# Performance work log

Measured on AMD Instinct MI355X. Metric: run time of the kernel, lower is better.

The kernel has to match this reference:

```python
import jax, jax.numpy as jnp
import numpy as np

PATCH = (1, 5, 5)   # NN_patch_size (t, h, w)
CHUNK = 3600


def unfold3d_patches(video):
    """video: [B,C,T,H,W] -> [N, d] overlapping (1,5,5) patches, stride 1, VALID.
    d = C*1*5*5; N = B*T*(H-4)*(W-4). Element order within d is consistent
    across calls, which is all the L2 KNN + MSE math requires."""
    p = jax.lax.conv_general_dilated_patches(
        video, filter_shape=PATCH, window_strides=(1, 1, 1), padding='VALID')
    # p: [B, C*prod(PATCH), T', H', W']
    d = p.shape[1]
    return jnp.moveaxis(p, 1, -1).reshape(-1, d)


def knn_argmin(q, k):
    """Exact 1-NN under L2 (faiss IndexFlatL2 equivalent), chunked over queries."""
    kn = jnp.sum(k * k, axis=1)                      # [Nk]
    qc = q.reshape(-1, CHUNK, q.shape[1])            # [nchunks, CHUNK, d]

    def one_chunk(qb):
        qn = jnp.sum(qb * qb, axis=1, keepdims=True)  # [CHUNK,1]
        d2 = qn + kn[None, :] - 2.0 * (qb @ k.T)      # [CHUNK, Nk]
        return jnp.argmin(d2, axis=1)

    return jax.lax.map(one_chunk, qc).reshape(-1)    # [Nq]


def setup_inputs() -> dict:
    key = jax.random.key(0)
    k1, k2 = jax.random.split(key)
    shape = (1, 3, 4, 64, 64)  # [B,C,T,H,W]
    return {
        'result': jax.random.normal(k1, shape, dtype=jnp.float32),
        'valid_video': jax.random.normal(k2, shape, dtype=jnp.float32),
    }


def reference(result, valid_video):
    q = unfold3d_patches(result)        # [Nq, 75] query patches
    k = unfold3d_patches(valid_video)   # [Nk, 75] valid (key/value) patches
    idx = knn_argmin(q, k)              # [Nq] nearest valid patch per query
    nn = k[idx]                         # gather (F.embedding equivalent)
    # nn.MSELoss(reduction='sum')
    diff = q - nn
    return jnp.sum(diff * diff)
```

## Files before the change

### kernel.cpp

```cpp
#include <hip/hip_runtime.h>
#include <hip/hip_bf16.h>
#include <math.h>

typedef __attribute__((ext_vector_type(8))) short bf16x8;
typedef __attribute__((ext_vector_type(4))) float f32x4;
typedef unsigned short ushort_t;

#define NP 14400
#define NS 5
#define NIT 45
#define TILEB 12288

__device__ __forceinline__ ushort_t f2bf(float f) {
  unsigned u = __float_as_uint(f);
  u += 0x7FFF + ((u >> 16) & 1);
  return (ushort_t)(u >> 16);
}
__device__ __forceinline__ float bf2f(ushort_t b) {
  return __uint_as_float(((unsigned)b) << 16);
}

__device__ __forceinline__ size_t kidx(int p, int d) {
  return ((size_t)(((p >> 6) * 12 + ((p >> 4) & 3) * 3 + (d >> 5)) * 64
          + ((d >> 3) & 3) * 16 + (p & 15))) * 8 + (d & 7);
}
__device__ __forceinline__ size_t qidx(int p, int d) {
  return ((size_t)(((p >> 4) * 3 + (d >> 5)) * 64
          + ((d >> 3) & 3) * 16 + (p & 15))) * 8 + (d & 7);
}

__global__ __launch_bounds__(256) void prep_kernel(
    const float* __restrict__ resv, const float* __restrict__ valv,
    ushort_t* __restrict__ Qb, ushort_t* __restrict__ Kb,
    float* __restrict__ qn, unsigned* __restrict__ rminb) {
  int w = threadIdx.x >> 6;
  int lane = threadIdx.x & 63;
  int pg = blockIdx.x * 4 + w;
  int isK = pg >= NP;
  int p = isK ? pg - NP : pg;
  const float* src = isK ? valv : resv;
  int t = p / 3600; int rem = p - t * 3600;
  int y = rem / 60;  int x = rem - y * 60;

  float v0, v1 = 0.f;
  {
    int d = lane;
    int c = d / 25; int r = d - c * 25; int dy = r / 5; int dx = r - dy * 5;
    v0 = src[((c * 4 + t) * 64 + (y + dy)) * 64 + (x + dx)];
  }
  if (lane < 11) {
    int d = lane + 64;
    int c = d / 25; int r = d - c * 25; int dy = r / 5; int dx = r - dy * 5;
    v1 = src[((c * 4 + t) * 64 + (y + dy)) * 64 + (x + dx)];
  }
  ushort_t b0 = f2bf(v0), b1 = f2bf(v1);
  float f0 = bf2f(b0), f1 = bf2f(b1);

  float sq = f0 * f0 + f1 * f1;
  #pragma unroll
  for (int off = 1; off < 64; off <<= 1) sq += __shfl_xor(sq, off, 64);

  if (isK) {
    ushort_t khi = f2bf(sq);
    ushort_t klo = f2bf(sq - bf2f(khi));
    ushort_t s1 = (lane < 11) ? b1
                : (lane == 11 ? khi : (lane == 12 ? klo : (ushort_t)0));
    Kb[kidx(p, lane)] = b0;
    if (lane < 32) Kb[kidx(p, lane + 64)] = s1;
  } else {
    ushort_t s0 = f2bf(-2.f * f0);
    ushort_t s1 = (lane < 11) ? f2bf(-2.f * f1)
                : ((lane == 11 || lane == 12) ? (ushort_t)0x3F80 : (ushort_t)0);
    Qb[qidx(p, lane)] = s0;
    if (lane < 32) Qb[qidx(p, lane + 64)] = s1;
    if (lane == 0) { qn[p] = sq; rminb[p] = 0xFFFFFFFFu; }
  }
}

__global__ __launch_bounds__(256, 4) void knn_kernel(
    const ushort_t* __restrict__ Qb, const ushort_t* __restrict__ Kb,
    unsigned* __restrict__ rminb) {
  int b = blockIdx.x;
  int xcd = b & 7, pos = b >> 3;
  int lin = (xcd < 5 ? xcd * 141 : 705 + (xcd - 5) * 140) + pos;
  int ns = lin / 225, rowblk = lin - ns * 225;
  int brow = rowblk * 64;
  int lane = threadIdx.x & 63;
  int w = threadIdx.x >> 6;
  int l15 = lane & 15, l4 = lane >> 4;

  const char* gW = (const char*)Kb + (size_t)(ns * 45) * TILEB
                   + w * 3072 + lane * 16;

  const char* Aw = (const char*)Qb + (size_t)(brow >> 4) * 3072 + lane * 16;
  bf16x8 af[4][3];
  #pragma unroll
  for (int rt = 0; rt < 4; ++rt)
    #pragma unroll
    for (int ks = 0; ks < 3; ++ks)
      af[rt][ks] = *(const bf16x8*)(Aw + (rt * 3 + ks) * 1024);

  float rmin[4][4];
  #pragma unroll
  for (int rt = 0; rt < 4; ++rt)
    #pragma unroll
    for (int j = 0; j < 4; ++j) rmin[rt][j] = INFINITY;

  const f32x4 fz = {0.f, 0.f, 0.f, 0.f};

  bf16x8 bbuf[2][3];

  auto loadB = [&](int bi, int it) {
    const char* g = gW + (size_t)it * TILEB;
    #pragma unroll
    for (int ks = 0; ks < 3; ++ks)
      bbuf[bi][ks] = *(const bf16x8*)(g + ks * 1024);
  };

  auto compute = [&](int bi) {
    f32x4 acc[4];
    {
      bf16x8 bv = bbuf[bi][0];
      #pragma unroll
      for (int rt = 0; rt < 4; ++rt)
        acc[rt] = __builtin_amdgcn_mfma_f32_16x16x32_bf16(af[rt][0], bv, fz, 0, 0, 0);
    }
    #pragma unroll
    for (int ks = 1; ks < 3; ++ks) {
      bf16x8 bv = bbuf[bi][ks];
      #pragma unroll
      for (int rt = 0; rt < 4; ++rt)
        acc[rt] = __builtin_amdgcn_mfma_f32_16x16x32_bf16(af[rt][ks], bv, acc[rt], 0, 0, 0);
    }
    #pragma unroll
    for (int rt = 0; rt < 4; ++rt)
      #pragma unroll
      for (int j = 0; j < 4; ++j)
        rmin[rt][j] = fminf(rmin[rt][j], acc[rt][j]);
  };

  loadB(0, 0);
  loadB(1, 1);

  int k = 0;
  #pragma unroll 1
  for (int tri = 0; tri < 21; ++tri, k += 2) {
    compute(0); loadB(0, k + 2);
    compute(1); loadB(1, k + 3);
  }
  compute(0); loadB(0, 44);
  compute(1);
  compute(0);

  #pragma unroll
  for (int rt = 0; rt < 4; ++rt)
    #pragma unroll
    for (int j = 0; j < 4; ++j) {
      float m = rmin[rt][j];
      m = fminf(m, __shfl_xor(m, 1, 64));
      m = fminf(m, __shfl_xor(m, 2, 64));
      m = fminf(m, __shfl_xor(m, 4, 64));
      m = fminf(m, __shfl_xor(m, 8, 64));
      if (l15 == 0) {
        unsigned bu = __float_as_uint(m);
        unsigned tu = bu ^ (unsigned)(((int)bu >> 31) | (int)0x80000000);
        atomicMin(&rminb[brow + rt * 16 + l4 * 4 + j], tu);
      }
    }
}

__global__ __launch_bounds__(64) void final1_kernel(
    const unsigned* __restrict__ rminb, const float* __restrict__ qn,
    float* __restrict__ partial) {
  int r = blockIdx.x * 64 + threadIdx.x;
  unsigned u = rminb[r];
  unsigned bu = (u & 0x80000000u) ? (u ^ 0x80000000u) : ~u;
  float val = __uint_as_float(bu) + qn[r];
  #pragma unroll
  for (int off = 32; off; off >>= 1) val += __shfl_down(val, off, 64);
  if (threadIdx.x == 0) partial[blockIdx.x] = val;
}

__global__ __launch_bounds__(256) void final2_kernel(
    const float* __restrict__ partial, float* __restrict__ out) {
  int t = threadIdx.x;
  float v = (t < 225) ? partial[t] : 0.f;
  #pragma unroll
  for (int off = 32; off; off >>= 1) v += __shfl_down(v, off, 64);
  __shared__ float s[4];
  if ((t & 63) == 0) s[t >> 6] = v;
  __syncthreads();
  if (t == 0) out[0] = s[0] + s[1] + s[2] + s[3];
}

extern "C" void kernel_launch(void* const* d_in, const int* in_sizes, int n_in,
                              void* d_out, int out_size, void* d_ws, size_t ws_size,
                              hipStream_t stream) {
  const float* resv = (const float*)d_in[0];
  const float* valv = (const float*)d_in[1];
  char* ws = (char*)d_ws;
  ushort_t* Qb    = (ushort_t*)ws;
  ushort_t* Kb    = (ushort_t*)(ws + 2764800);
  float* qn       = (float*)(ws + 5529600);
  unsigned* rminb = (unsigned*)(ws + 5587200);
  float* partial  = (float*)(ws + 5644800);
  float* out = (float*)d_out;

  prep_kernel<<<7200, 256, 0, stream>>>(resv, valv, Qb, Kb, qn, rminb);
  knn_kernel<<<1125, 256, 0, stream>>>(Qb, Kb, rminb);
  final1_kernel<<<225, 64, 0, stream>>>(rminb, qn, partial);
  final2_kernel<<<1, 256, 0, stream>>>(partial, out);
}
```

Before: 55.10 us.

## Fuse final reduction into KNN kernel, repartition keys into 4 splits with padding

Pads the key set to 14592 rows with dummy patches whose norm term is huge, so the keys split into 4 slices of 57 tiles instead of 5 of 45. This gives 900 blocks, which fit in a single wave at 4 blocks per CU. The two final reduction kernels are replaced by a last-block-done pattern using an atomic counter inside the KNN kernel, removing two launches. It also raises wave priority around the MFMA sequence. The trade-off is longer per-block loops and a serial final reduction done by one block.

```diff
diff --git a/kernel.cpp b/kernel.cpp
--- a/kernel.cpp
+++ b/kernel.cpp
@@ -7,8 +7,9 @@
 typedef unsigned short ushort_t;
 
 #define NP 14400
-#define NS 5
-#define NIT 45
+#define NPK 14592
+#define NS 4
+#define NIT 57
 #define TILEB 12288
 
 __device__ __forceinline__ ushort_t f2bf(float f) {
@@ -32,12 +33,22 @@
 __global__ __launch_bounds__(256) void prep_kernel(
     const float* __restrict__ resv, const float* __restrict__ valv,
     ushort_t* __restrict__ Qb, ushort_t* __restrict__ Kb,
-    float* __restrict__ qn, unsigned* __restrict__ rminb) {
+    float* __restrict__ qn, unsigned* __restrict__ rminb,
+    unsigned* __restrict__ counter) {
   int w = threadIdx.x >> 6;
   int lane = threadIdx.x & 63;
   int pg = blockIdx.x * 4 + w;
+  if (pg == 0 && lane == 0) *counter = 0;
   int isK = pg >= NP;
   int p = isK ? pg - NP : pg;
+
+  if (isK && p >= NP) {
+    Kb[kidx(p, lane)] = 0;
+    if (lane < 32)
+      Kb[kidx(p, lane + 64)] = (lane == 11) ? (ushort_t)0x7F7F : (ushort_t)0;
+    return;
+  }
+
   const float* src = isK ? valv : resv;
   int t = p / 3600; int rem = p - t * 3600;
   int y = rem / 60;  int x = rem - y * 60;
@@ -79,17 +90,18 @@
 
 __global__ __launch_bounds__(256, 4) void knn_kernel(
     const ushort_t* __restrict__ Qb, const ushort_t* __restrict__ Kb,
-    unsigned* __restrict__ rminb) {
+    unsigned* __restrict__ rminb, const float* __restrict__ qn,
+    unsigned* __restrict__ counter, float* __restrict__ out) {
   int b = blockIdx.x;
   int xcd = b & 7, pos = b >> 3;
-  int lin = (xcd < 5 ? xcd * 141 : 705 + (xcd - 5) * 140) + pos;
+  int lin = (xcd < 4 ? xcd * 113 : 452 + (xcd - 4) * 112) + pos;
   int ns = lin / 225, rowblk = lin - ns * 225;
   int brow = rowblk * 64;
   int lane = threadIdx.x & 63;
   int w = threadIdx.x >> 6;
   int l15 = lane & 15, l4 = lane >> 4;
 
-  const char* gW = (const char*)Kb + (size_t)(ns * 45) * TILEB
+  const char* gW = (const char*)Kb + (size_t)(ns * NIT) * TILEB
                    + w * 3072 + lane * 16;
 
   const char* Aw = (const char*)Qb + (size_t)(brow >> 4) * 3072 + lane * 16;
@@ -119,6 +131,7 @@
 
   auto compute = [&](int bi) {
     f32x4 acc[4];
+    __builtin_amdgcn_s_setprio(1);
     {
       bf16x8 bv = bbuf[bi][0];
       #pragma unroll
@@ -132,6 +145,7 @@
       for (int rt = 0; rt < 4; ++rt)
         acc[rt] = __builtin_amdgcn_mfma_f32_16x16x32_bf16(af[rt][ks], bv, acc[rt], 0, 0, 0);
     }
+    __builtin_amdgcn_s_setprio(0);
     #pragma unroll
     for (int rt = 0; rt < 4; ++rt)
       #pragma unroll
@@ -144,11 +158,11 @@
 
   int k = 0;
   #pragma unroll 1
-  for (int tri = 0; tri < 21; ++tri, k += 2) {
+  for (int tri = 0; tri < 27; ++tri, k += 2) {
     compute(0); loadB(0, k + 2);
     compute(1); loadB(1, k + 3);
   }
-  compute(0); loadB(0, 44);
+  compute(0); loadB(0, 56);
   compute(1);
   compute(0);
 
@@ -167,30 +181,28 @@
         atomicMin(&rminb[brow + rt * 16 + l4 * 4 + j], tu);
       }
     }
-}
-
-__global__ __launch_bounds__(64) void final1_kernel(
-    const unsigned* __restrict__ rminb, const float* __restrict__ qn,
-    float* __restrict__ partial) {
-  int r = blockIdx.x * 64 + threadIdx.x;
-  unsigned u = rminb[r];
-  unsigned bu = (u & 0x80000000u) ? (u ^ 0x80000000u) : ~u;
-  float val = __uint_as_float(bu) + qn[r];
-  #pragma unroll
-  for (int off = 32; off; off >>= 1) val += __shfl_down(val, off, 64);
-  if (threadIdx.x == 0) partial[blockIdx.x] = val;
-}
-
-__global__ __launch_bounds__(256) void final2_kernel(
-    const float* __restrict__ partial, float* __restrict__ out) {
-  int t = threadIdx.x;
-  float v = (t < 225) ? partial[t] : 0.f;
-  #pragma unroll
-  for (int off = 32; off; off >>= 1) v += __shfl_down(v, off, 64);
-  __shared__ float s[4];
-  if ((t & 63) == 0) s[t >> 6] = v;
+
+  __threadfence();
+  __shared__ unsigned amLast;
+  if (threadIdx.x == 0) amLast = (atomicAdd(counter, 1) == 899u);
   __syncthreads();
-  if (t == 0) out[0] = s[0] + s[1] + s[2] + s[3];
+  if (!amLast) return;
+  __threadfence();
+
+  const volatile unsigned* rv = (const volatile unsigned*)rminb;
+  int tid = threadIdx.x;
+  float s = 0.f;
+  for (int i = tid; i < NP; i += 256) {
+    unsigned u = rv[i];
+    unsigned bu = (u & 0x80000000u) ? (u ^ 0x80000000u) : ~u;
+    s += __uint_as_float(bu) + qn[i];
+  }
+  #pragma unroll
+  for (int off = 32; off; off >>= 1) s += __shfl_down(s, off, 64);
+  __shared__ float red[4];
+  if ((tid & 63) == 0) red[tid >> 6] = s;
+  __syncthreads();
+  if (tid == 0) out[0] = red[0] + red[1] + red[2] + red[3];
 }
 
 extern "C" void kernel_launch(void* const* d_in, const int* in_sizes, int n_in,
@@ -199,15 +211,13 @@
   const float* resv = (const float*)d_in[0];
   const float* valv = (const float*)d_in[1];
   char* ws = (char*)d_ws;
-  ushort_t* Qb    = (ushort_t*)ws;
-  ushort_t* Kb    = (ushort_t*)(ws + 2764800);
-  float* qn       = (float*)(ws + 5529600);
-  unsigned* rminb = (unsigned*)(ws + 5587200);
-  float* partial  = (float*)(ws + 5644800);
+  ushort_t* Qb      = (ushort_t*)ws;
+  ushort_t* Kb      = (ushort_t*)(ws + 2764800);
+  float* qn         = (float*)(ws + 5566464);
+  unsigned* rminb   = (unsigned*)(ws + 5624064);
+  unsigned* counter = (unsigned*)(ws + 5681664);
   float* out = (float*)d_out;
 
-  prep_kernel<<<7200, 256, 0, stream>>>(resv, valv, Qb, Kb, qn, rminb);
-  knn_kernel<<<1125, 256, 0, stream>>>(Qb, Kb, rminb);
-  final1_kernel<<<225, 64, 0, stream>>>(rminb, qn, partial);
-  final2_kernel<<<1, 256, 0, stream>>>(partial, out);
-}
+  prep_kernel<<<7248, 256, 0, stream>>>(resv, valv, Qb, Kb, qn, rminb, counter);
+  knn_kernel<<<900, 256, 0, stream>>>(Qb, Kb, rminb, qn, counter, out);
+}
```

Result: slower. 131.0 us (+137.7%).
